# Kernel optimization log

Hardware: AMD Instinct MI355X
Metric: run time of the kernel (lower is better)

Reference implementation:

```python
import jax, jax.numpy as jnp
import numpy as np

N = 8192       # nodes
E = 262144     # edges (avg degree 32)
IN_DIM, HID, EMB = 512, 256, 64


def setup_inputs() -> dict:
    key = jax.random.key(0)
    ks = jax.random.split(key, 7)
    features = jax.random.normal(ks[0], (N, IN_DIM), dtype=jnp.float32)
    edge_index = jax.random.randint(ks[1], (2, E), 0, N, dtype=jnp.int32)
    edge_weight = jax.random.uniform(ks[2], (E,), dtype=jnp.float32)
    W0 = jax.random.normal(ks[3], (IN_DIM, HID), dtype=jnp.float32) * (1.0 / np.sqrt(IN_DIM))
    W_mean = jax.random.normal(ks[4], (HID, EMB), dtype=jnp.float32) * (1.0 / np.sqrt(HID))
    W_logstd = jax.random.normal(ks[5], (HID, EMB), dtype=jnp.float32) * (1.0 / np.sqrt(HID))
    noise = jax.random.normal(ks[6], (N, EMB), dtype=jnp.float32)
    return {"features": features, "edge_index": edge_index, "edge_weight": edge_weight,
            "W0": W0, "W_mean": W_mean, "W_logstd": W_logstd, "noise": noise}


def reference(features, edge_index, edge_weight, W0, W_mean, W_logstd, noise):
    src, dst = edge_index[0], edge_index[1]
    n = features.shape[0]

    def gcn(x, W):
        h = x @ W                                   # dense transform first (smaller dim)
        msg = h[src] * edge_weight[:, None]         # gather + weight
        return jax.ops.segment_sum(msg, dst, num_segments=n)  # scatter-add aggregate

    hidden = gcn(features, W0)                       # [N, HID] (gcn_base, no activation)
    mean = jax.nn.relu(gcn(hidden, W_mean))          # [N, EMB]
    logstd = jax.nn.relu(gcn(hidden, W_logstd))      # [N, EMB]
    Z = noise * jnp.exp(logstd) + mean               # reparameterization
    adj_logits = Z @ Z.T                             # [N, N] inner-product decoder
    return adj_logits
```

## Files before the change

kernel.cpp:

```cpp
#include <hip/hip_runtime.h>
#include <hip/hip_bf16.h>

#define N_NODES 8192
#define N_EDGES 262144
#define IN_DIM  512
#define HID     256
#define EMB     64
#define C2      128

__global__ __launch_bounds__(256) void k_count(const int* __restrict__ dst, int* __restrict__ deg) {
    int e = blockIdx.x * 256 + threadIdx.x;
    atomicAdd(&deg[dst[e]], 1);
}

__global__ __launch_bounds__(1024) void k_scan(const int* __restrict__ deg, int* __restrict__ rowptr) {
    __shared__ int part[1024];
    const int t = threadIdx.x;
    const int base = t * 8;
    int v[8], incl[8];
    int s = 0;
    #pragma unroll
    for (int j = 0; j < 8; ++j) { v[j] = deg[base + j]; s += v[j]; incl[j] = s; }
    part[t] = s;
    __syncthreads();
    for (int off = 1; off < 1024; off <<= 1) {
        int x = (t >= off) ? part[t - off] : 0;
        __syncthreads();
        part[t] += x;
        __syncthreads();
    }
    int excl = part[t] - s;
    if (t == 0) rowptr[0] = 0;
    #pragma unroll
    for (int j = 0; j < 8; ++j) rowptr[base + j + 1] = excl + incl[j];
}

__global__ __launch_bounds__(256) void k_fill(const int* __restrict__ src, const int* __restrict__ dst,
                                              const float* __restrict__ ew, const int* __restrict__ rowptr,
                                              int* __restrict__ cursor, int* __restrict__ srcs,
                                              float* __restrict__ wsorted) {
    int e = blockIdx.x * 256 + threadIdx.x;
    int d = dst[e];
    int p = rowptr[d] + atomicAdd(&cursor[d], 1);
    srcs[p] = src[e];
    wsorted[p] = ew[e];
}

__global__ __launch_bounds__(256) void k_wc(const float* __restrict__ W0, const float* __restrict__ Wm,
                                            const float* __restrict__ Wl, float* __restrict__ WcT) {
    __shared__ float w0s[16][256];
    const int t = threadIdx.x;
    const int kb = blockIdx.x * 16;
    #pragma unroll
    for (int m = 0; m < 4; ++m) {
        int f = t + 256 * m;
        int row = f >> 6, q = f & 63;
        *(float4*)&w0s[row][q * 4] = *(const float4*)&W0[(size_t)(kb + row) * 256 + q * 4];
    }
    __syncthreads();
    const int j = t & 127, kh = t >> 7;
    const float* B = (j < 64) ? (Wm + j) : (Wl + (j - 64));
    float acc[8] = {};
    for (int h = 0; h < 256; h += 4) {
        float b0 = B[(h + 0) * 64], b1 = B[(h + 1) * 64];
        float b2 = B[(h + 2) * 64], b3 = B[(h + 3) * 64];
        #pragma unroll
        for (int r = 0; r < 8; ++r) {
            float4 x = *(const float4*)&w0s[kh * 8 + r][h];
            acc[r] += x.x * b0 + x.y * b1 + x.z * b2 + x.w * b3;
        }
    }
    #pragma unroll
    for (int r = 0; r < 8; ++r)
        WcT[(size_t)j * 512 + kb + kh * 8 + r] = acc[r];
}

__global__ __launch_bounds__(256) void k_gemm_p(const float* __restrict__ X, const float* __restrict__ WcT,
                                                float* __restrict__ P) {
    __shared__ float Xs[32][68];
    const int t = threadIdx.x;
    const int i0 = blockIdx.x * 32;
    const int rg = t >> 6, cpair = t & 63, c0 = cpair * 2;
    float acc[8][2] = {};
    for (int kc = 0; kc < 512; kc += 64) {
        #pragma unroll
        for (int m = 0; m < 2; ++m) {
            int f = t + 256 * m;
            int row = f >> 4, q = f & 15;
            *(float4*)&Xs[row][q * 4] = *(const float4*)&X[(size_t)(i0 + row) * 512 + kc + q * 4];
        }
        __syncthreads();
        #pragma unroll 4
        for (int k4 = 0; k4 < 16; ++k4) {
            float4 wA = *(const float4*)&WcT[(size_t)c0 * 512 + kc + k4 * 4];
            float4 wB = *(const float4*)&WcT[(size_t)(c0 + 1) * 512 + kc + k4 * 4];
            #pragma unroll
            for (int r = 0; r < 8; ++r) {
                float4 x = *(const float4*)&Xs[rg * 8 + r][k4 * 4];
                acc[r][0] += x.x * wA.x + x.y * wA.y + x.z * wA.z + x.w * wA.w;
                acc[r][1] += x.x * wB.x + x.y * wB.y + x.z * wB.z + x.w * wB.w;
            }
        }
        __syncthreads();
    }
    #pragma unroll
    for (int r = 0; r < 8; ++r) {
        float2 v = make_float2(acc[r][0], acc[r][1]);
        *(float2*)&P[(size_t)(i0 + rg * 8 + r) * 128 + c0] = v;
    }
}

__global__ __launch_bounds__(128) void k_agg(const float* __restrict__ In, const int* __restrict__ rowptr,
                                             const int* __restrict__ srcs, const float* __restrict__ wsorted,
                                             float* __restrict__ Out, const float* __restrict__ noise,
                                             float* __restrict__ Z, int zpass) {
    const int b = blockIdx.x, t = threadIdx.x;
    const int beg = rowptr[b], end = rowptr[b + 1];
    float a0 = 0.f, a1 = 0.f, a2 = 0.f, a3 = 0.f;
    int i = beg;
    for (; i + 4 <= end; i += 4) {
        int   s0 = srcs[i],     s1 = srcs[i + 1], s2 = srcs[i + 2], s3 = srcs[i + 3];
        float w0 = wsorted[i],  w1 = wsorted[i + 1], w2 = wsorted[i + 2], w3 = wsorted[i + 3];
        a0 += In[(size_t)s0 * C2 + t] * w0;
        a1 += In[(size_t)s1 * C2 + t] * w1;
        a2 += In[(size_t)s2 * C2 + t] * w2;
        a3 += In[(size_t)s3 * C2 + t] * w3;
    }
    for (; i < end; ++i)
        a0 += In[(size_t)srcs[i] * C2 + t] * wsorted[i];
    float acc = (a0 + a1) + (a2 + a3);
    if (!zpass) {
        Out[(size_t)b * C2 + t] = acc;
    } else {
        __shared__ float u[C2];
        u[t] = acc;
        __syncthreads();
        if (t < 64) {
            float m = fmaxf(u[t], 0.f);
            float l = fmaxf(u[t + 64], 0.f);
            float z = noise[(size_t)b * 64 + t] * expf(fminf(l, 80.f)) + m;
            z = fminf(fmaxf(z, -1e18f), 1e18f);
            Z[(size_t)b * 64 + t] = z;
        }
    }
}

__global__ __launch_bounds__(256) void k_zzt(const float* __restrict__ Z, float* __restrict__ out) {
    if (blockIdx.x < blockIdx.y) return;
    __shared__ float Ta[64][68];
    __shared__ float Tb[64][68];
    const int t = threadIdx.x;
    const int i0 = blockIdx.y * 64, j0 = blockIdx.x * 64;
    #pragma unroll
    for (int m = 0; m < 4; ++m) {
        int f = t + 256 * m;
        int row = f >> 4, q = f & 15;
        float4 va = *(const float4*)&Z[(size_t)(i0 + row) * 64 + q * 4];
        float4 vb = *(const float4*)&Z[(size_t)(j0 + row) * 64 + q * 4];
        int k = q * 4;
        Ta[k + 0][row] = va.x; Ta[k + 1][row] = va.y; Ta[k + 2][row] = va.z; Ta[k + 3][row] = va.w;
        Tb[k + 0][row] = vb.x; Tb[k + 1][row] = vb.y; Tb[k + 2][row] = vb.z; Tb[k + 3][row] = vb.w;
    }
    __syncthreads();
    const int tx = t & 15, ty = t >> 4;
    float acc[4][4] = {};
    #pragma unroll 8
    for (int k = 0; k < 64; ++k) {
        float4 a = *(const float4*)&Ta[k][ty * 4];
        float4 b = *(const float4*)&Tb[k][tx * 4];
        acc[0][0] += a.x * b.x; acc[0][1] += a.x * b.y; acc[0][2] += a.x * b.z; acc[0][3] += a.x * b.w;
        acc[1][0] += a.y * b.x; acc[1][1] += a.y * b.y; acc[1][2] += a.y * b.z; acc[1][3] += a.y * b.w;
        acc[2][0] += a.z * b.x; acc[2][1] += a.z * b.y; acc[2][2] += a.z * b.z; acc[2][3] += a.z * b.w;
        acc[3][0] += a.w * b.x; acc[3][1] += a.w * b.y; acc[3][2] += a.w * b.z; acc[3][3] += a.w * b.w;
    }
    #pragma unroll
    for (int r = 0; r < 4; ++r) {
        float4 v = make_float4(acc[r][0], acc[r][1], acc[r][2], acc[r][3]);
        *(float4*)&out[(size_t)(i0 + ty * 4 + r) * N_NODES + j0 + tx * 4] = v;
    }
    if (i0 != j0) {
        __syncthreads();
        #pragma unroll
        for (int r = 0; r < 4; ++r)
            #pragma unroll
            for (int c = 0; c < 4; ++c)
                Ta[tx * 4 + c][ty * 4 + r] = acc[r][c];
        __syncthreads();
        #pragma unroll
        for (int m = 0; m < 4; ++m) {
            int f = t + 256 * m;
            int row = f >> 4, q = f & 15;
            float4 v = *(const float4*)&Ta[row][q * 4];
            *(float4*)&out[(size_t)(j0 + row) * N_NODES + i0 + q * 4] = v;
        }
    }
}

extern "C" void kernel_launch(void* const* d_in, const int* in_sizes, int n_in,
                              void* d_out, int out_size, void* d_ws, size_t ws_size,
                              hipStream_t stream) {
    const float* X     = (const float*)d_in[0];
    const int*   ei    = (const int*)d_in[1];
    const float* ew    = (const float*)d_in[2];
    const float* W0    = (const float*)d_in[3];
    const float* Wm    = (const float*)d_in[4];
    const float* Wl    = (const float*)d_in[5];
    const float* noise = (const float*)d_in[6];
    float* out = (float*)d_out;

    const int* srcI = ei;
    const int* dstI = ei + N_EDGES;

    int*   deg     = (int*)d_ws;
    int*   cursor  = deg + 8192;
    int*   rowptr  = deg + 16384;
    int*   srcs    = deg + 24592;
    float* wsorted = (float*)(deg + 24592 + N_EDGES);
    float* WcT     = wsorted + N_EDGES;
    float* P       = WcT + 128 * 512;
    float* U1      = P + (size_t)N_NODES * C2;
    float* Z       = U1 + (size_t)N_NODES * C2;

    hipMemsetAsync(deg, 0, 16384 * sizeof(int), stream);

    k_count<<<N_EDGES / 256, 256, 0, stream>>>(dstI, deg);
    k_scan<<<1, 1024, 0, stream>>>(deg, rowptr);
    k_fill<<<N_EDGES / 256, 256, 0, stream>>>(srcI, dstI, ew, rowptr, cursor, srcs, wsorted);
    k_wc<<<32, 256, 0, stream>>>(W0, Wm, Wl, WcT);
    k_gemm_p<<<N_NODES / 32, 256, 0, stream>>>(X, WcT, P);
    k_agg<<<N_NODES, 128, 0, stream>>>(P, rowptr, srcs, wsorted, U1, nullptr, nullptr, 0);
    k_agg<<<N_NODES, 128, 0, stream>>>(U1, rowptr, srcs, wsorted, nullptr, noise, Z, 1);
    k_zzt<<<dim3(N_NODES / 64, N_NODES / 64), 256, 0, stream>>>(Z, out);
}
```

Measured before the change: 470.9 us.

## Enlarge ZZ^T tiles to 128x128 and drop shared-memory staging

The Z·Zᵀ kernel now computes 128x128 output tiles, with each thread holding an 8x8 accumulator block. Operands are read straight from global memory as float4 along k, so the LDS transpose staging and its barriers are gone. The mirrored lower-triangle tile is written directly from registers as float4 columns, with no shared-memory transpose. This cuts the launch count and the per-tile overhead for the write-bound 256MB output. In exchange it raises register pressure and relies on the cache for repeated global loads of Z, and the transposed stores from each thread go to scattered rows.

```diff
diff --git a/kernel.cpp b/kernel.cpp
--- a/kernel.cpp
+++ b/kernel.cpp
@@ -147,52 +147,59 @@
 
 __global__ __launch_bounds__(256) void k_zzt(const float* __restrict__ Z, float* __restrict__ out) {
     if (blockIdx.x < blockIdx.y) return;
-    __shared__ float Ta[64][68];
-    __shared__ float Tb[64][68];
-    const int t = threadIdx.x;
-    const int i0 = blockIdx.y * 64, j0 = blockIdx.x * 64;
-    #pragma unroll
-    for (int m = 0; m < 4; ++m) {
-        int f = t + 256 * m;
-        int row = f >> 4, q = f & 15;
-        float4 va = *(const float4*)&Z[(size_t)(i0 + row) * 64 + q * 4];
-        float4 vb = *(const float4*)&Z[(size_t)(j0 + row) * 64 + q * 4];
-        int k = q * 4;
-        Ta[k + 0][row] = va.x; Ta[k + 1][row] = va.y; Ta[k + 2][row] = va.z; Ta[k + 3][row] = va.w;
-        Tb[k + 0][row] = vb.x; Tb[k + 1][row] = vb.y; Tb[k + 2][row] = vb.z; Tb[k + 3][row] = vb.w;
-    }
-    __syncthreads();
+    const int t = threadIdx.x;
     const int tx = t & 15, ty = t >> 4;
-    float acc[4][4] = {};
-    #pragma unroll 8
-    for (int k = 0; k < 64; ++k) {
-        float4 a = *(const float4*)&Ta[k][ty * 4];
-        float4 b = *(const float4*)&Tb[k][tx * 4];
-        acc[0][0] += a.x * b.x; acc[0][1] += a.x * b.y; acc[0][2] += a.x * b.z; acc[0][3] += a.x * b.w;
-        acc[1][0] += a.y * b.x; acc[1][1] += a.y * b.y; acc[1][2] += a.y * b.z; acc[1][3] += a.y * b.w;
-        acc[2][0] += a.z * b.x; acc[2][1] += a.z * b.y; acc[2][2] += a.z * b.z; acc[2][3] += a.z * b.w;
-        acc[3][0] += a.w * b.x; acc[3][1] += a.w * b.y; acc[3][2] += a.w * b.z; acc[3][3] += a.w * b.w;
-    }
-    #pragma unroll
-    for (int r = 0; r < 4; ++r) {
-        float4 v = make_float4(acc[r][0], acc[r][1], acc[r][2], acc[r][3]);
-        *(float4*)&out[(size_t)(i0 + ty * 4 + r) * N_NODES + j0 + tx * 4] = v;
-    }
+    const int i0 = blockIdx.y * 128, j0 = blockIdx.x * 128;
+    const float* A0 = Z + (size_t)(i0 + ty * 4) * 64;
+    const float* A1 = Z + (size_t)(i0 + 64 + ty * 4) * 64;
+    const float* B0 = Z + (size_t)(j0 + tx * 4) * 64;
+    const float* B1 = Z + (size_t)(j0 + 64 + tx * 4) * 64;
+    float acc[2][4][2][4] = {};
+    for (int k = 0; k < 64; k += 4) {
+        float4 a[2][4], b[2][4];
+        #pragma unroll
+        for (int r = 0; r < 4; ++r) {
+            a[0][r] = *(const float4*)&A0[r * 64 + k];
+            a[1][r] = *(const float4*)&A1[r * 64 + k];
+            b[0][r] = *(const float4*)&B0[r * 64 + k];
+            b[1][r] = *(const float4*)&B1[r * 64 + k];
+        }
+        #pragma unroll
+        for (int rg = 0; rg < 2; ++rg)
+            #pragma unroll
+            for (int r = 0; r < 4; ++r)
+                #pragma unroll
+                for (int cg = 0; cg < 2; ++cg)
+                    #pragma unroll
+                    for (int c = 0; c < 4; ++c)
+                        acc[rg][r][cg][c] += a[rg][r].x * b[cg][c].x + a[rg][r].y * b[cg][c].y
+                                           + a[rg][r].z * b[cg][c].z + a[rg][r].w * b[cg][c].w;
+    }
+    #pragma unroll
+    for (int rg = 0; rg < 2; ++rg)
+        #pragma unroll
+        for (int r = 0; r < 4; ++r) {
+            size_t row = (size_t)(i0 + rg * 64 + ty * 4 + r);
+            #pragma unroll
+            for (int cg = 0; cg < 2; ++cg) {
+                float4 v = make_float4(acc[rg][r][cg][0], acc[rg][r][cg][1],
+                                       acc[rg][r][cg][2], acc[rg][r][cg][3]);
+                *(float4*)&out[row * N_NODES + j0 + cg * 64 + tx * 4] = v;
+            }
+        }
     if (i0 != j0) {
-        __syncthreads();
-        #pragma unroll
-        for (int r = 0; r < 4; ++r)
-            #pragma unroll
-            for (int c = 0; c < 4; ++c)
-                Ta[tx * 4 + c][ty * 4 + r] = acc[r][c];
-        __syncthreads();
-        #pragma unroll
-        for (int m = 0; m < 4; ++m) {
-            int f = t + 256 * m;
-            int row = f >> 4, q = f & 15;
-            float4 v = *(const float4*)&Ta[row][q * 4];
-            *(float4*)&out[(size_t)(j0 + row) * N_NODES + i0 + q * 4] = v;
-        }
+        #pragma unroll
+        for (int cg = 0; cg < 2; ++cg)
+            #pragma unroll
+            for (int c = 0; c < 4; ++c) {
+                size_t row = (size_t)(j0 + cg * 64 + tx * 4 + c);
+                #pragma unroll
+                for (int rg = 0; rg < 2; ++rg) {
+                    float4 v = make_float4(acc[rg][0][cg][c], acc[rg][1][cg][c],
+                                           acc[rg][2][cg][c], acc[rg][3][cg][c]);
+                    *(float4*)&out[row * N_NODES + i0 + rg * 64 + ty * 4] = v;
+                }
+            }
     }
 }
 
@@ -230,5 +237,5 @@
     k_gemm_p<<<N_NODES / 32, 256, 0, stream>>>(X, WcT, P);
     k_agg<<<N_NODES, 128, 0, stream>>>(P, rowptr, srcs, wsorted, U1, nullptr, nullptr, 0);
     k_agg<<<N_NODES, 128, 0, stream>>>(U1, rowptr, srcs, wsorted, nullptr, noise, Z, 1);
-    k_zzt<<<dim3(N_NODES / 64, N_NODES / 64), 256, 0, stream>>>(Z, out);
-}
+    k_zzt<<<dim3(N_NODES / 128, N_NODES / 128), 256, 0, stream>>>(Z, out);
+}
```

Measured after the change: 640.9 us. +36.1%, slower.
